# Kernel optimization log

Hardware: AMD Instinct MI355X
Metric: run time of the kernel (lower is better)

Reference implementation:

```python
import jax, jax.numpy as jnp
import numpy as np

L1, L2, B = 512, 512, 2
D1, D2, BN = 256, 256, 256
NEG = jnp.float32(-1e12)


def setup_inputs() -> dict:
    key = jax.random.key(0)
    ks = jax.random.split(key, 8)
    s = 0.05
    return {
        "ctx_1": jax.random.normal(ks[0], (L1, B, D1), jnp.float32),
        "ctx_2": jax.random.normal(ks[1], (L2, B, D2), jnp.float32),
        "ctx_1_mask": jnp.ones((L1, B), jnp.float32),
        "ctx_2_mask": jnp.ones((L2, B), jnp.float32),
        # mlp_hid: Conv2d(D1+D2 -> BN, 1x1) with bias
        "Wh": jax.random.normal(ks[2], (D1 + D2, BN), jnp.float32) * s,
        "bh": jnp.zeros((BN,), jnp.float32),
        # mlp_out: Conv2d(BN -> 1, 1x1), bias=False (mlp_bias default)
        "wo": jax.random.normal(ks[3], (BN,), jnp.float32) * s,
        # project_1_to_2 / project_2_to_1: Linear(D1+D2 -> BN) with bias
        "W12": jax.random.normal(ks[4], (D2 + D1, BN), jnp.float32) * s,
        "b12": jnp.zeros((BN,), jnp.float32),
        "W21": jax.random.normal(ks[5], (D1 + D2, BN), jnp.float32) * s,
        "b21": jnp.zeros((BN,), jnp.float32),
    }


def reference(ctx_1, ctx_2, ctx_1_mask, ctx_2_mask, Wh, bh, wo, W12, b12, W21, b21):
    d1 = ctx_1.shape[-1]
    # 1x1 conv on cat([b_ctx_1, b_ctx_2]) == sum of two independent projections
    Wh1, Wh2 = Wh[:d1], Wh[d1:]
    p1 = jnp.einsum('lbd,dk->blk', ctx_1, Wh1)            # (B, L1, K)
    p2 = jnp.einsum('mbd,dk->bmk', ctx_2, Wh2)            # (B, L2, K)
    hidden = jnp.tanh(p1[:, :, None, :] + p2[:, None, :, :] + bh)  # (B, L1, L2, K)
    affinity = jnp.einsum('blmk,k->blm', hidden, wo)      # (B, L1, L2)
    # masked in both directions
    affinity = affinity + (1.0 - ctx_1_mask.T)[:, :, None] * NEG
    affinity = affinity + (1.0 - ctx_2_mask.T)[:, None, :] * NEG
    # 1 -> 2 direction: softmax over L2
    dist_1_to_2 = jax.nn.softmax(affinity, axis=2)        # (B, L1, L2)
    context_1_to_2 = jnp.einsum('lbd,blm->mbd', ctx_1, dist_1_to_2)  # (L2, B, D1)
    seq_1_to_2 = jnp.tanh(jnp.concatenate([ctx_2, context_1_to_2], axis=-1) @ W12 + b12)
    # 2 -> 1 direction: softmax over L1 (then contracted over L2, as in the torch code)
    dist_2_to_1 = jax.nn.softmax(affinity, axis=1)        # (B, L1, L2)
    context_2_to_1 = jnp.einsum('mbd,blm->lbd', ctx_2, dist_2_to_1)  # (L1, B, D2)
    seq_2_to_1 = jnp.tanh(jnp.concatenate([ctx_1, context_2_to_1], axis=-1) @ W21 + b21)
    return (seq_2_to_1, seq_1_to_2)
```

## Files before the change

### kernel.cpp

```cpp
#include <hip/hip_runtime.h>


#define NEGC (-1e12f)
#define TWO_LOG2E 2.8853900817779268f
#define LOG2E 1.4426950408889634f
#define N2LOG2E (-2.8853900817779268f)

typedef __attribute__((ext_vector_type(8))) short bf16x8;
typedef __attribute__((ext_vector_type(4))) float f32x4;

__device__ __forceinline__ short f2bf(float x)
{
    union { float f; unsigned u; } v; v.f = x;
    unsigned r = (v.u + 0x7FFFu + ((v.u >> 16) & 1u)) >> 16;
    return (short)r;
}

__global__ __launch_bounds__(256) void k_proj(
    const float* __restrict__ ctx1, const float* __restrict__ ctx2,
    const float* __restrict__ Wh, const float* __restrict__ bh,
    const float* __restrict__ W12, const float* __restrict__ b12,
    const float* __restrict__ W21, const float* __restrict__ b21,
    const float* __restrict__ mask1, const float* __restrict__ mask2,
    float* __restrict__ E1, float* __restrict__ E2,
    float* __restrict__ P12, float* __restrict__ U1,
    float* __restrict__ P21, float* __restrict__ U2,
    float* __restrict__ p1, float* __restrict__ p2,
    float* __restrict__ S1, float* __restrict__ S2)
{
    const int t  = threadIdx.x;
    const int g  = blockIdx.z;
    const int r0 = blockIdx.x * 64;
    const int n0 = blockIdx.y * 64;

    const float* A; const float* W; const float* bias; int expm; float* outp;
    switch (g) {
      case 0:  A=ctx1; W=Wh;        bias=bh;   expm=1; outp=E1;  break;
      case 1:  A=ctx2; W=Wh+65536;  bias=0;    expm=1; outp=E2;  break;
      case 2:  A=ctx2; W=W12;       bias=b12;  expm=0; outp=P12; break;
      case 3:  A=ctx1; W=W12+65536; bias=0;    expm=0; outp=U1;  break;
      case 4:  A=ctx1; W=W21;       bias=b21;  expm=0; outp=P21; break;
      default: A=ctx2; W=W21+65536; bias=0;    expm=0; outp=U2;  break;
    }

    if (g == 0 && blockIdx.x == 0 && blockIdx.y == 0) {
        for (int idx = t; idx < 1024; idx += 256) {
            int row = idx >> 1, b = idx & 1;
            p1[b * 512 + row] = __builtin_amdgcn_exp2f(LOG2E * (1.f - mask1[idx]) * NEGC);
            p2[b * 512 + row] = __builtin_amdgcn_exp2f(LOG2E * (1.f - mask2[idx]) * NEGC);
            S1[b * 512 + row] = 0.f;
            S2[b * 512 + row] = 0.f;
        }
    }

    __shared__ __align__(16) short Abf[64 * 136];
    __shared__ __align__(16) short Bbf[64 * 136];

    const int w    = t >> 6;
    const int lane = t & 63;
    const int quad = lane >> 4;
    const int lr   = lane & 15;

    f32x4 acc[4] = {};

    for (int kc = 0; kc < 256; kc += 128) {
        #pragma unroll
        for (int i = 0; i < 8; ++i) {
            int slot = i * 256 + t;
            int r = slot >> 5, kq = (slot & 31) << 2;
            float4 v = *(const float4*)(A + (r0 + r) * 256 + kc + kq);
            short4 s; s.x = f2bf(v.x); s.y = f2bf(v.y); s.z = f2bf(v.z); s.w = f2bf(v.w);
            *(short4*)(Abf + r * 136 + kq) = s;
        }
        #pragma unroll
        for (int i = 0; i < 8; ++i) {
            int slot = i * 256 + t;
            int bk = slot >> 4, bn4 = (slot & 15) << 2;
            float4 v = *(const float4*)(W + (kc + bk) * 256 + n0 + bn4);
            Bbf[(bn4 + 0) * 136 + bk] = f2bf(v.x);
            Bbf[(bn4 + 1) * 136 + bk] = f2bf(v.y);
            Bbf[(bn4 + 2) * 136 + bk] = f2bf(v.z);
            Bbf[(bn4 + 3) * 136 + bk] = f2bf(v.w);
        }
        __syncthreads();
        #pragma unroll
        for (int s = 0; s < 4; ++s) {
            const int kb = s * 32 + quad * 8;
            bf16x8 a = *(const bf16x8*)(Abf + (w * 16 + lr) * 136 + kb);
            #pragma unroll
            for (int nc = 0; nc < 4; ++nc) {
                bf16x8 b = *(const bf16x8*)(Bbf + (nc * 16 + lr) * 136 + kb);
                acc[nc] = __builtin_amdgcn_mfma_f32_16x16x32_bf16(a, b, acc[nc], 0, 0, 0);
            }
        }
        __syncthreads();
    }

    #pragma unroll
    for (int nc = 0; nc < 4; ++nc) {
        const int col = n0 + nc * 16 + lr;
        const float bv = bias ? bias[col] : 0.f;
        #pragma unroll
        for (int reg = 0; reg < 4; ++reg) {
            int row  = r0 + w * 16 + quad * 4 + reg;
            int orow = ((row & 1) << 9) + (row >> 1);
            float v = acc[nc][reg] + bv;
            if (expm) v = __builtin_amdgcn_exp2f(v * TWO_LOG2E);
            outp[orow * 256 + col] = v;
        }
    }
}

#define PAIR(AV, QV, WV, ACC) do {                                    \
    float x0_ = fmaf(AV.x, QV.x, 1.f);                                \
    float x1_ = fmaf(AV.y, QV.y, 1.f);                                \
    float x2_ = fmaf(AV.z, QV.z, 1.f);                                \
    float x3_ = fmaf(AV.w, QV.w, 1.f);                                \
    float r01_ = __builtin_amdgcn_rcpf(x0_ * x1_);                    \
    float r23_ = __builtin_amdgcn_rcpf(x2_ * x3_);                    \
    float z01_ = fmaf(WV.y, x0_, WV.x * x1_);                         \
    float z23_ = fmaf(WV.w, x2_, WV.z * x3_);                         \
    ACC = fmaf(r01_, z01_, ACC);                                      \
    ACC = fmaf(r23_, z23_, ACC);                                      \
} while (0)

__global__ __launch_bounds__(256) void k_aff(
    const float* __restrict__ E1g, const float* __restrict__ E2g,
    const float* __restrict__ wo,
    const float* __restrict__ p1g, const float* __restrict__ p2g,
    float* __restrict__ EN, float* __restrict__ ET,
    float* __restrict__ S1, float* __restrict__ S2)
{
    const int t  = threadIdx.x;
    const int l0 = blockIdx.x * 32, m0 = blockIdx.y * 32, b = blockIdx.z;

    __shared__ __align__(16) float E1s[32 * 132];
    __shared__ __align__(16) float E2s[32 * 132];
    __shared__ __align__(16) float affs[32 * 36];

    const int tl = t >> 4, tm = t & 15;
    float acc[2][2] = {};

    for (int kc = 0; kc < 256; kc += 128) {
        #pragma unroll
        for (int i = 0; i < 4; ++i) {
            int slot = i * 256 + t;
            int r = slot >> 5, kq = (slot & 31) << 2;
            *(float4*)(E1s + r * 132 + kq) =
                *(const float4*)(E1g + (((b << 9) + l0 + r) << 8) + kc + kq);
            *(float4*)(E2s + r * 132 + kq) =
                *(const float4*)(E2g + (((b << 9) + m0 + r) << 8) + kc + kq);
        }
        __syncthreads();
        #pragma unroll 4
        for (int k0 = 0; k0 < 128; k0 += 4) {
            const float4 w  = *(const float4*)(wo + kc + k0);
            const float4 a0 = *(const float4*)(E1s + tl * 132 + k0);
            const float4 a1 = *(const float4*)(E1s + (tl + 16) * 132 + k0);
            const float4 q0 = *(const float4*)(E2s + tm * 132 + k0);
            const float4 q1 = *(const float4*)(E2s + (tm + 16) * 132 + k0);
            PAIR(a0, q0, w, acc[0][0]);
            PAIR(a0, q1, w, acc[0][1]);
            PAIR(a1, q0, w, acc[1][0]);
            PAIR(a1, q1, w, acc[1][1]);
        }
        __syncthreads();
    }

    affs[tl * 36 + tm]             = __builtin_amdgcn_exp2f(acc[0][0] * N2LOG2E);
    affs[tl * 36 + tm + 16]        = __builtin_amdgcn_exp2f(acc[0][1] * N2LOG2E);
    affs[(tl + 16) * 36 + tm]      = __builtin_amdgcn_exp2f(acc[1][0] * N2LOG2E);
    affs[(tl + 16) * 36 + tm + 16] = __builtin_amdgcn_exp2f(acc[1][1] * N2LOG2E);
    __syncthreads();

    const int r  = t >> 3;
    const int c4 = (t & 7) << 2;
    {
        float4 e = *(const float4*)(affs + r * 36 + c4);
        const float p1r = p1g[(b << 9) + l0 + r];
        float4 vn = make_float4(e.x * p1r, e.y * p1r, e.z * p1r, e.w * p1r);
        *(float4*)(EN + (((b << 9) + l0 + r) << 9) + m0 + c4) = vn;
        float4 p2v = *(const float4*)(p2g + (b << 9) + m0 + c4);
        float s = (e.x * p2v.x + e.y * p2v.y) + (e.z * p2v.z + e.w * p2v.w);
        s += __shfl_xor(s, 1, 64);
        s += __shfl_xor(s, 2, 64);
        s += __shfl_xor(s, 4, 64);
        if ((t & 7) == 0) atomicAdd(S1 + (b << 9) + l0 + r, s);
    }
    {
        float4 te;
        te.x = affs[(c4 + 0) * 36 + r];
        te.y = affs[(c4 + 1) * 36 + r];
        te.z = affs[(c4 + 2) * 36 + r];
        te.w = affs[(c4 + 3) * 36 + r];
        const float p2r = p2g[(b << 9) + m0 + r];
        float4 vt = make_float4(te.x * p2r, te.y * p2r, te.z * p2r, te.w * p2r);
        *(float4*)(ET + (((b << 9) + m0 + r) << 9) + l0 + c4) = vt;
        float4 p1v = *(const float4*)(p1g + (b << 9) + l0 + c4);
        float s = (te.x * p1v.x + te.y * p1v.y) + (te.z * p1v.z + te.w * p1v.w);
        s += __shfl_xor(s, 1, 64);
        s += __shfl_xor(s, 2, 64);
        s += __shfl_xor(s, 4, 64);
        if ((t & 7) == 0) atomicAdd(S2 + (b << 9) + m0 + r, s);
    }
}

__global__ __launch_bounds__(256) void k_final(
    const float* __restrict__ EN, const float* __restrict__ ET,
    const float* __restrict__ U1, const float* __restrict__ U2,
    const float* __restrict__ P12, const float* __restrict__ P21,
    const float* __restrict__ S1, const float* __restrict__ S2,
    float* __restrict__ out)
{
    const int t   = threadIdx.x;
    const int r0  = blockIdx.x * 32, n0 = blockIdx.y * 32;
    const int dir = blockIdx.z >> 1, b = blockIdx.z & 1;
    const float* Ag = (dir == 0 ? ET  : EN)  + b * 262144;
    const float* Sg = (dir == 0 ? S1  : S2)  + b * 512;
    const float* Bg = (dir == 0 ? U1  : U2)  + b * 131072;
    const float* Pg = (dir == 0 ? P12 : P21) + b * 131072;
    float* o = out + (dir == 0 ? 262144 : 0);

    __shared__ __align__(16) short Abf[32 * 72];
    __shared__ __align__(16) short Bbf[32 * 72];
    __shared__ __align__(16) float rs[512];

    for (int i = t; i < 512; i += 256)
        rs[i] = __builtin_amdgcn_rcpf(Sg[i]);
    __syncthreads();

    const int w    = t >> 6;
    const int lane = t & 63;
    const int quad = lane >> 4;
    const int lr   = lane & 15;
    const int wr   = (w >> 1) << 4, wc = (w & 1) << 4;
    f32x4 acc = {};

    for (int kc = 0; kc < 512; kc += 64) {
        #pragma unroll
        for (int i = 0; i < 2; ++i) {
            int slot = i * 256 + t;
            int r = slot >> 4, kq = (slot & 15) << 2;
            float4 v = *(const float4*)(Ag + ((r0 + r) << 9) + kc + kq);
            const float* rp = rs + kc + kq;
            short4 s;
            s.x = f2bf(v.x * rp[0]); s.y = f2bf(v.y * rp[1]);
            s.z = f2bf(v.z * rp[2]); s.w = f2bf(v.w * rp[3]);
            *(short4*)(Abf + r * 72 + kq) = s;
        }
        #pragma unroll
        for (int i = 0; i < 2; ++i) {
            int slot = i * 256 + t;
            int bk = slot >> 3, bn4 = (slot & 7) << 2;
            float4 v = *(const float4*)(Bg + ((kc + bk) << 8) + n0 + bn4);
            Bbf[(bn4 + 0) * 72 + bk] = f2bf(v.x);
            Bbf[(bn4 + 1) * 72 + bk] = f2bf(v.y);
            Bbf[(bn4 + 2) * 72 + bk] = f2bf(v.z);
            Bbf[(bn4 + 3) * 72 + bk] = f2bf(v.w);
        }
        __syncthreads();
        #pragma unroll
        for (int s = 0; s < 2; ++s) {
            const int kb = s * 32 + quad * 8;
            bf16x8 a = *(const bf16x8*)(Abf + (wr + lr) * 72 + kb);
            bf16x8 bb = *(const bf16x8*)(Bbf + (wc + lr) * 72 + kb);
            acc = __builtin_amdgcn_mfma_f32_16x16x32_bf16(a, bb, acc, 0, 0, 0);
        }
        __syncthreads();
    }

    const int col = n0 + wc + lr;
    #pragma unroll
    for (int reg = 0; reg < 4; ++reg) {
        const int m = r0 + wr + quad * 4 + reg;
        float v = acc[reg] + Pg[(m << 8) + col];
        float tv = 1.f - 2.f * __builtin_amdgcn_rcpf(
                       __builtin_amdgcn_exp2f(v * TWO_LOG2E) + 1.f);
        o[((m << 1) + b) * 256 + col] = tv;
    }
}

extern "C" void kernel_launch(void* const* d_in, const int* in_sizes, int n_in,
                              void* d_out, int out_size, void* d_ws, size_t ws_size,
                              hipStream_t stream)
{
    const float* ctx1 = (const float*)d_in[0];
    const float* ctx2 = (const float*)d_in[1];
    const float* m1   = (const float*)d_in[2];
    const float* m2   = (const float*)d_in[3];
    const float* Wh   = (const float*)d_in[4];
    const float* bh   = (const float*)d_in[5];
    const float* wo   = (const float*)d_in[6];
    const float* W12  = (const float*)d_in[7];
    const float* b12  = (const float*)d_in[8];
    const float* W21  = (const float*)d_in[9];
    const float* b21  = (const float*)d_in[10];
    float* out = (float*)d_out;
    float* ws  = (float*)d_ws;

    float* E1  = ws;
    float* E2  = E1  + 262144;
    float* P12 = E2  + 262144;
    float* U1  = P12 + 262144;
    float* P21 = U1  + 262144;
    float* U2  = P21 + 262144;
    float* p1  = U2  + 262144;
    float* p2  = p1  + 1024;
    float* S1  = p2  + 1024;
    float* S2  = S1  + 1024;
    float* EN  = S2  + 1024;
    float* ET  = EN  + 524288;

    hipLaunchKernelGGL(k_proj, dim3(16, 4, 6), dim3(256), 0, stream,
                       ctx1, ctx2, Wh, bh, W12, b12, W21, b21, m1, m2,
                       E1, E2, P12, U1, P21, U2, p1, p2, S1, S2);
    hipLaunchKernelGGL(k_aff, dim3(16, 16, 2), dim3(256), 0, stream,
                       E1, E2, wo, p1, p2, EN, ET, S1, S2);
    hipLaunchKernelGGL(k_final, dim3(16, 8, 4), dim3(256), 0, stream,
                       EN, ET, U1, U2, P12, P21, S1, S2, out);
}
```

Before: 118.8 us.

## Pre-transpose weights to bf16 and load MFMA operands directly from global

Adds a prep kernel that converts the weight matrices to bf16 and transposes them into an n-major layout, so the projection GEMM can read B fragments straight from global memory. The projection kernel drops its LDS staging and barriers: it loads A fragments from global, converts them in registers and feeds MFMA directly. The aim is to remove the strided LDS transpose writes and the synchronisation. In exchange it adds an extra kernel launch and relies on uncoalesced, cache-dependent global fragment reads.

```diff
diff --git a/kernel.cpp b/kernel.cpp
--- a/kernel.cpp
+++ b/kernel.cpp
@@ -16,34 +16,28 @@
     return (short)r;
 }
 
-__global__ __launch_bounds__(256) void k_proj(
-    const float* __restrict__ ctx1, const float* __restrict__ ctx2,
-    const float* __restrict__ Wh, const float* __restrict__ bh,
-    const float* __restrict__ W12, const float* __restrict__ b12,
-    const float* __restrict__ W21, const float* __restrict__ b21,
+__global__ __launch_bounds__(256) void k_prep(
+    const float* __restrict__ Wh, const float* __restrict__ W12,
+    const float* __restrict__ W21,
     const float* __restrict__ mask1, const float* __restrict__ mask2,
-    float* __restrict__ E1, float* __restrict__ E2,
-    float* __restrict__ P12, float* __restrict__ U1,
-    float* __restrict__ P21, float* __restrict__ U2,
+    short* __restrict__ Wt,
     float* __restrict__ p1, float* __restrict__ p2,
     float* __restrict__ S1, float* __restrict__ S2)
 {
-    const int t  = threadIdx.x;
-    const int g  = blockIdx.z;
-    const int r0 = blockIdx.x * 64;
-    const int n0 = blockIdx.y * 64;
-
-    const float* A; const float* W; const float* bias; int expm; float* outp;
+    const int t = threadIdx.x, bx = blockIdx.x;
+    const int g = bx >> 4, tile = bx & 15;
+    const int tk = (tile >> 2) * 64, tn = (tile & 3) * 64;
+    const float* Wsrc; int rbase;
     switch (g) {
-      case 0:  A=ctx1; W=Wh;        bias=bh;   expm=1; outp=E1;  break;
-      case 1:  A=ctx2; W=Wh+65536;  bias=0;    expm=1; outp=E2;  break;
-      case 2:  A=ctx2; W=W12;       bias=b12;  expm=0; outp=P12; break;
-      case 3:  A=ctx1; W=W12+65536; bias=0;    expm=0; outp=U1;  break;
-      case 4:  A=ctx1; W=W21;       bias=b21;  expm=0; outp=P21; break;
-      default: A=ctx2; W=W21+65536; bias=0;    expm=0; outp=U2;  break;
-    }
-
-    if (g == 0 && blockIdx.x == 0 && blockIdx.y == 0) {
+      case 0:  Wsrc = Wh;  rbase = 0;   break;
+      case 1:  Wsrc = Wh;  rbase = 256; break;
+      case 2:  Wsrc = W12; rbase = 0;   break;
+      case 3:  Wsrc = W12; rbase = 256; break;
+      case 4:  Wsrc = W21; rbase = 0;   break;
+      default: Wsrc = W21; rbase = 256; break;
+    }
+
+    if (bx == 0) {
         for (int idx = t; idx < 1024; idx += 256) {
             int row = idx >> 1, b = idx & 1;
             p1[b * 512 + row] = __builtin_amdgcn_exp2f(LOG2E * (1.f - mask1[idx]) * NEGC);
@@ -53,47 +47,73 @@
         }
     }
 
-    __shared__ __align__(16) short Abf[64 * 136];
-    __shared__ __align__(16) short Bbf[64 * 136];
+    __shared__ __align__(16) float Ls[64 * 68];
+    #pragma unroll
+    for (int i = 0; i < 4; ++i) {
+        int slot = i * 256 + t;
+        int r = slot >> 4, c4 = (slot & 15) << 2;
+        *(float4*)(Ls + r * 68 + c4) =
+            *(const float4*)(Wsrc + (rbase + tk + r) * 256 + tn + c4);
+    }
+    __syncthreads();
+    #pragma unroll
+    for (int i = 0; i < 4; ++i) {
+        int slot = i * 256 + t;
+        int n = slot >> 4, k4 = (slot & 15) << 2;
+        short4 s;
+        s.x = f2bf(Ls[(k4 + 0) * 68 + n]);
+        s.y = f2bf(Ls[(k4 + 1) * 68 + n]);
+        s.z = f2bf(Ls[(k4 + 2) * 68 + n]);
+        s.w = f2bf(Ls[(k4 + 3) * 68 + n]);
+        *(short4*)(Wt + g * 65536 + (tn + n) * 256 + tk + k4) = s;
+    }
+}
+
+__global__ __launch_bounds__(256) void k_proj(
+    const float* __restrict__ ctx1, const float* __restrict__ ctx2,
+    const short* __restrict__ Wt,
+    const float* __restrict__ bh, const float* __restrict__ b12,
+    const float* __restrict__ b21,
+    float* __restrict__ E1, float* __restrict__ E2,
+    float* __restrict__ P12, float* __restrict__ U1,
+    float* __restrict__ P21, float* __restrict__ U2)
+{
+    const int t  = threadIdx.x;
+    const int g  = blockIdx.z;
+    const int r0 = blockIdx.x * 64;
+    const int n0 = blockIdx.y * 64;
+
+    const float* A; const float* bias; int expm; float* outp;
+    switch (g) {
+      case 0:  A=ctx1; bias=bh;   expm=1; outp=E1;  break;
+      case 1:  A=ctx2; bias=0;    expm=1; outp=E2;  break;
+      case 2:  A=ctx2; bias=b12;  expm=0; outp=P12; break;
+      case 3:  A=ctx1; bias=0;    expm=0; outp=U1;  break;
+      case 4:  A=ctx1; bias=b21;  expm=0; outp=P21; break;
+      default: A=ctx2; bias=0;    expm=0; outp=U2;  break;
+    }
 
     const int w    = t >> 6;
     const int lane = t & 63;
     const int quad = lane >> 4;
     const int lr   = lane & 15;
 
+    const float* ap = A + (r0 + w * 16 + lr) * 256 + quad * 8;
+    const short* bp = Wt + g * 65536 + (n0 + lr) * 256 + quad * 8;
+
     f32x4 acc[4] = {};
-
-    for (int kc = 0; kc < 256; kc += 128) {
-        #pragma unroll
-        for (int i = 0; i < 8; ++i) {
-            int slot = i * 256 + t;
-            int r = slot >> 5, kq = (slot & 31) << 2;
-            float4 v = *(const float4*)(A + (r0 + r) * 256 + kc + kq);
-            short4 s; s.x = f2bf(v.x); s.y = f2bf(v.y); s.z = f2bf(v.z); s.w = f2bf(v.w);
-            *(short4*)(Abf + r * 136 + kq) = s;
-        }
-        #pragma unroll
-        for (int i = 0; i < 8; ++i) {
-            int slot = i * 256 + t;
-            int bk = slot >> 4, bn4 = (slot & 15) << 2;
-            float4 v = *(const float4*)(W + (kc + bk) * 256 + n0 + bn4);
-            Bbf[(bn4 + 0) * 136 + bk] = f2bf(v.x);
-            Bbf[(bn4 + 1) * 136 + bk] = f2bf(v.y);
-            Bbf[(bn4 + 2) * 136 + bk] = f2bf(v.z);
-            Bbf[(bn4 + 3) * 136 + bk] = f2bf(v.w);
-        }
-        __syncthreads();
-        #pragma unroll
-        for (int s = 0; s < 4; ++s) {
-            const int kb = s * 32 + quad * 8;
-            bf16x8 a = *(const bf16x8*)(Abf + (w * 16 + lr) * 136 + kb);
-            #pragma unroll
-            for (int nc = 0; nc < 4; ++nc) {
-                bf16x8 b = *(const bf16x8*)(Bbf + (nc * 16 + lr) * 136 + kb);
-                acc[nc] = __builtin_amdgcn_mfma_f32_16x16x32_bf16(a, b, acc[nc], 0, 0, 0);
-            }
-        }
-        __syncthreads();
+    #pragma unroll
+    for (int kc = 0; kc < 256; kc += 32) {
+        float4 v0 = *(const float4*)(ap + kc);
+        float4 v1 = *(const float4*)(ap + kc + 4);
+        bf16x8 a;
+        a[0] = f2bf(v0.x); a[1] = f2bf(v0.y); a[2] = f2bf(v0.z); a[3] = f2bf(v0.w);
+        a[4] = f2bf(v1.x); a[5] = f2bf(v1.y); a[6] = f2bf(v1.z); a[7] = f2bf(v1.w);
+        #pragma unroll
+        for (int nc = 0; nc < 4; ++nc) {
+            bf16x8 b = *(const bf16x8*)(bp + nc * 4096 + kc);
+            acc[nc] = __builtin_amdgcn_mfma_f32_16x16x32_bf16(a, b, acc[nc], 0, 0, 0);
+        }
     }
 
     #pragma unroll
@@ -310,10 +330,13 @@
     float* S2  = S1  + 1024;
     float* EN  = S2  + 1024;
     float* ET  = EN  + 524288;
-
+    short* Wt  = (short*)(ET + 524288);
+
+    hipLaunchKernelGGL(k_prep, dim3(96), dim3(256), 0, stream,
+                       Wh, W12, W21, m1, m2, Wt, p1, p2, S1, S2);
     hipLaunchKernelGGL(k_proj, dim3(16, 4, 6), dim3(256), 0, stream,
-                       ctx1, ctx2, Wh, bh, W12, b12, W21, b21, m1, m2,
-                       E1, E2, P12, U1, P21, U2, p1, p2, S1, S2);
+                       ctx1, ctx2, Wt, bh, b12, b21,
+                       E1, E2, P12, U1, P21, U2);
     hipLaunchKernelGGL(k_aff, dim3(16, 16, 2), dim3(256), 0, stream,
                        E1, E2, wo, p1, p2, EN, ET, S1, S2);
     hipLaunchKernelGGL(k_final, dim3(16, 8, 4), dim3(256), 0, stream,
```

Result: slower. 122.1 us (+2.8%).
